# Kernel tuning notes

Measured on AMD Instinct MI355X. Metric: run time of the kernel, lower is better.

The kernel has to match this reference:

```python
import jax, jax.numpy as jnp
import numpy as np
from jax.ops import segment_sum

N_NODES = 50000
N_EDGES = 800000
D = 64
N_LAYERS = 3
N_GRAPHS = 512


def setup_inputs() -> dict:
    key = jax.random.key(0)
    k1, k2, k3, k4 = jax.random.split(key, 4)
    x = jax.random.normal(k1, (N_NODES, D), dtype=jnp.float32)
    Ws = jax.random.normal(k2, (N_LAYERS, D, D), dtype=jnp.float32) * (1.0 / np.sqrt(D))
    bs = jnp.zeros((N_LAYERS, D), dtype=jnp.float32)
    edge_index = jax.random.randint(k3, (2, N_EDGES), 0, N_NODES, dtype=jnp.int64)
    batch = jnp.sort(jax.random.randint(k4, (N_NODES,), 0, N_GRAPHS, dtype=jnp.int64))
    return {"x": x, "Ws": Ws, "bs": bs, "edge_index": edge_index, "batch": batch}


def _gcn_layer(h, W, b, src, dst, n_nodes, dinv):
    # h: [N, D] -> linear transform then normalized aggregation (PyG GCNConv,
    # add_self_loops=True, symmetric normalization)
    h = h @ W  # [N, D]
    norm = dinv[src] * dinv[dst]  # [E]
    agg = segment_sum(h[src] * norm[:, None], dst, num_segments=n_nodes)
    # self-loop contribution: norm_ii = dinv[i]^2, weight 1
    agg = agg + h * (dinv * dinv)[:, None]
    return agg + b


def reference(x, Ws, bs, edge_index, batch):
    src, dst = edge_index[0], edge_index[1]
    n_nodes = x.shape[0]
    # degree with self-loops (edge weight 1): deg[i] = in-degree + 1
    deg = segment_sum(jnp.ones((src.shape[0],), dtype=x.dtype), dst,
                      num_segments=n_nodes) + 1.0
    dinv = jax.lax.rsqrt(deg)
    h = x
    for l in range(Ws.shape[0]):
        h = _gcn_layer(h, Ws[l], bs[l], src, dst, n_nodes, dinv)
    # global_mean_pool over batch index
    sums = segment_sum(h, batch, num_segments=N_GRAPHS)  # [G, D]
    counts = segment_sum(jnp.ones((n_nodes,), dtype=h.dtype), batch,
                         num_segments=N_GRAPHS)
    return sums / jnp.maximum(counts, 1.0)[:, None]
```

## Files before the change

kernel.cpp:

```cpp
#include <hip/hip_runtime.h>

#define N_NODES 50000
#define N_EDGES 800000
#define D 64
#define N_LAYERS 3
#define N_GRAPHS 512

#define NB 196
#define BCAP 5120
#define P3_CHUNK 2048
#define N_P3_WG ((N_EDGES + P3_CHUNK - 1) / P3_CHUNK)
#define LPAD 68

__global__ __launch_bounds__(256) void gbounds_kernel(
    const int* __restrict__ batch, int* __restrict__ gstart,
    int* __restrict__ bucket_fill, int nN) {
    int i = blockIdx.x * 256 + threadIdx.x;
    if (blockIdx.x == 0 && threadIdx.x < NB) bucket_fill[threadIdx.x] = 0;
    if (i >= nN) return;
    int b = batch[i];
    int prev = (i == 0) ? -1 : batch[i - 1];
    for (int g = prev + 1; g <= b; ++g) gstart[g] = i;
    if (i == nN - 1) {
        for (int g = b + 1; g <= N_GRAPHS; ++g) gstart[g] = nN;
    }
}


__global__ __launch_bounds__(256) void bucket_scatter_kernel(
    const int* __restrict__ src, const int* __restrict__ dst,
    int* __restrict__ bucket_fill, int* __restrict__ bucketArr, int nE) {
    __shared__ int hist[NB], base[NB], cur[NB];
    int tid = threadIdx.x;
    if (tid < NB) hist[tid] = 0;
    __syncthreads();
    int s8[8], d8[8];
    bool v8[8];
    int ebase = blockIdx.x * P3_CHUNK + tid;
    #pragma unroll
    for (int i = 0; i < 8; ++i) {
        int e = ebase + i * 256;
        v8[i] = (e < nE);
        if (v8[i]) {
            s8[i] = src[e];
            d8[i] = dst[e];
            atomicAdd(&hist[d8[i] >> 8], 1);
        }
    }
    __syncthreads();
    if (tid < NB) {
        base[tid] = atomicAdd(&bucket_fill[tid], hist[tid]);
        cur[tid] = 0;
    }
    __syncthreads();
    #pragma unroll
    for (int i = 0; i < 8; ++i) {
        if (v8[i]) {
            int b = d8[i] >> 8;
            int r = atomicAdd(&cur[b], 1);
            int pos = base[b] + r;
            if (pos < BCAP)
                bucketArr[b * BCAP + pos] = (s8[i] & 0xFFFF) | ((d8[i] & 0xFF) << 16);
        }
    }
}

__global__ __launch_bounds__(256) void bucket_csr_kernel(
    const int* __restrict__ bucket_fill, const int* __restrict__ bucketArr,
    const float* __restrict__ x,
    int* __restrict__ offsets, int* __restrict__ csr_src,
    float* __restrict__ dinv, float* __restrict__ v0) {
    __shared__ int bsum[256];
    __shared__ int ldeg[256], lsc[256], lcur[256];
    int b = blockIdx.x;
    int tid = threadIdx.x;
    int ownb = (tid < NB) ? bucket_fill[tid] : 0;
    bsum[tid] = ownb;
    __syncthreads();
    for (int off = 1; off < 256; off <<= 1) {
        int v = (tid >= off) ? bsum[tid - off] : 0;
        __syncthreads();
        bsum[tid] += v;
        __syncthreads();
    }
    int cbase = (b == 0) ? 0 : bsum[b - 1];
    if (b == NB - 1 && tid == 0) offsets[N_NODES] = bsum[NB - 1];
    int cnt = min(bucket_fill[b], BCAP);
    const int* seg = bucketArr + b * BCAP;
    ldeg[tid] = 0;
    __syncthreads();
    for (int e = tid; e < cnt; e += 256)
        atomicAdd(&ldeg[(seg[e] >> 16) & 0xFF], 1);
    __syncthreads();
    int own = ldeg[tid];
    lsc[tid] = own;
    __syncthreads();
    for (int off = 1; off < 256; off <<= 1) {
        int v = (tid >= off) ? lsc[tid - off] : 0;
        __syncthreads();
        lsc[tid] += v;
        __syncthreads();
    }
    int excl = lsc[tid] - own;
    int node = b * 256 + tid;
    if (node < N_NODES) {
        float di = rsqrtf((float)own + 1.0f);
        offsets[node] = cbase + excl;
        dinv[node] = di;
        const float4* xr = (const float4*)&x[(size_t)node * D];
        float4* vr = (float4*)&v0[(size_t)node * D];
        #pragma unroll
        for (int i = 0; i < D / 4; ++i) {
            float4 t = xr[i];
            t.x *= di; t.y *= di; t.z *= di; t.w *= di;
            vr[i] = t;
        }
    }
    lcur[tid] = cbase + excl;
    __syncthreads();
    for (int e = tid; e < cnt; e += 256) {
        int p = seg[e];
        int pos = atomicAdd(&lcur[(p >> 16) & 0xFF], 1);
        csr_src[pos] = p & 0xFFFF;
    }
}

__global__ __launch_bounds__(256) void fused_layer_kernel(
    const int* __restrict__ offsets, const int* __restrict__ csr_src,
    const float* __restrict__ v, const float* __restrict__ dinv,
    const float* __restrict__ W, const float* __restrict__ b,
    float* __restrict__ vout, int last) {
    __shared__ float A[16][LPAD];
    __shared__ float Wl[D][LPAD];
    int tid = threadIdx.x;
    #pragma unroll
    for (int i = 0; i < 4; ++i) {
        int idx4 = tid + i * 256;
        int r = idx4 >> 4;
        int c4 = (idx4 & 15) << 2;
        *(float4*)&Wl[r][c4] = *(const float4*)&W[r * D + c4];
    }
    int wave = tid >> 6;
    int lane = tid & 63;
    int grp = lane >> 4;
    int q4  = (lane & 15) << 2;
    int t0 = blockIdx.x * 16;
    #pragma unroll
    for (int rr = 0; rr < 4; ++rr) {
        int r = rr * 4 + wave;
        int t = t0 + r;
        int beg = offsets[t];
        int end = offsets[t + 1];
        float4 acc0 = make_float4(0.f, 0.f, 0.f, 0.f);
        float4 acc1 = make_float4(0.f, 0.f, 0.f, 0.f);
        int e = beg + grp;
        for (; e + 4 < end; e += 8) {
            int s0 = csr_src[e];
            int s1 = csr_src[e + 4];
            float4 v0 = *(const float4*)&v[(size_t)s0 * D + q4];
            float4 v1 = *(const float4*)&v[(size_t)s1 * D + q4];
            acc0.x += v0.x; acc0.y += v0.y; acc0.z += v0.z; acc0.w += v0.w;
            acc1.x += v1.x; acc1.y += v1.y; acc1.z += v1.z; acc1.w += v1.w;
        }
        if (e < end) {
            int s0 = csr_src[e];
            float4 v0 = *(const float4*)&v[(size_t)s0 * D + q4];
            acc0.x += v0.x; acc0.y += v0.y; acc0.z += v0.z; acc0.w += v0.w;
        }
        float4 acc = make_float4(acc0.x + acc1.x, acc0.y + acc1.y,
                                 acc0.z + acc1.z, acc0.w + acc1.w);
        #pragma unroll
        for (int m = 16; m < 64; m <<= 1) {
            acc.x += __shfl_xor(acc.x, m);
            acc.y += __shfl_xor(acc.y, m);
            acc.z += __shfl_xor(acc.z, m);
            acc.w += __shfl_xor(acc.w, m);
        }
        if (grp == 0) {
            float4 self = *(const float4*)&v[(size_t)t * D + q4];
            float dt = dinv[t];
            float4 a;
            a.x = (acc.x + self.x) * dt;
            a.y = (acc.y + self.y) * dt;
            a.z = (acc.z + self.z) * dt;
            a.w = (acc.w + self.w) * dt;
            *(float4*)&A[r][q4] = a;
        }
    }
    __syncthreads();
    int r  = tid >> 4;
    int c0 = (tid & 15) << 2;
    float4 acc = make_float4(0.f, 0.f, 0.f, 0.f);
    #pragma unroll
    for (int k = 0; k < D; k += 4) {
        float4 a  = *(float4*)&A[r][k];
        float4 w0 = *(float4*)&Wl[k + 0][c0];
        float4 w1 = *(float4*)&Wl[k + 1][c0];
        float4 w2 = *(float4*)&Wl[k + 2][c0];
        float4 w3 = *(float4*)&Wl[k + 3][c0];
        acc.x += a.x * w0.x + a.y * w1.x + a.z * w2.x + a.w * w3.x;
        acc.y += a.x * w0.y + a.y * w1.y + a.z * w2.y + a.w * w3.y;
        acc.z += a.x * w0.z + a.y * w1.z + a.z * w2.z + a.w * w3.z;
        acc.w += a.x * w0.w + a.y * w1.w + a.z * w2.w + a.w * w3.w;
    }
    int t = t0 + r;
    float4 bb = *(const float4*)&b[c0];
    float4 o;
    o.x = acc.x + bb.x;
    o.y = acc.y + bb.y;
    o.z = acc.z + bb.z;
    o.w = acc.w + bb.w;
    if (!last) {
        float dt = dinv[t];
        o.x *= dt; o.y *= dt; o.z *= dt; o.w *= dt;
    }
    *(float4*)&vout[(size_t)t * D + c0] = o;
}


__global__ __launch_bounds__(256) void pool_kernel(
    const float* __restrict__ h, const int* __restrict__ gstart,
    float* __restrict__ out) {
    __shared__ float sm[4][D];
    int g = blockIdx.x;
    int wave = threadIdx.x >> 6;
    int lane = threadIdx.x & 63;
    int beg = gstart[g];
    int end = gstart[g + 1];
    float acc = 0.f;
    int n = beg + wave;
    for (; n + 12 < end; n += 16) {
        float a0 = h[(size_t)(n)      * D + lane];
        float a1 = h[(size_t)(n + 4)  * D + lane];
        float a2 = h[(size_t)(n + 8)  * D + lane];
        float a3 = h[(size_t)(n + 12) * D + lane];
        acc += a0 + a1 + a2 + a3;
    }
    for (; n < end; n += 4)
        acc += h[(size_t)n * D + lane];
    sm[wave][lane] = acc;
    __syncthreads();
    if (wave == 0) {
        float s = sm[0][lane] + sm[1][lane] + sm[2][lane] + sm[3][lane];
        float cnt = (float)(end - beg);
        out[g * D + lane] = s / fmaxf(cnt, 1.0f);
    }
}


#define WS_ALIGN(p) ((char*)(((size_t)(p) + 255) & ~(size_t)255))

extern "C" void kernel_launch(void* const* d_in, const int* in_sizes, int n_in,
                              void* d_out, int out_size, void* d_ws, size_t ws_size,
                              hipStream_t stream) {
    const float* x     = (const float*)d_in[0];
    const float* Ws    = (const float*)d_in[1];
    const float* bs    = (const float*)d_in[2];
    const int*   edge  = (const int*)d_in[3];
    const int*   batch = (const int*)d_in[4];
    const int* src = edge;
    const int* dst = edge + N_EDGES;
    float* out = (float*)d_out;

    char* p = (char*)d_ws;
    int* offsets     = (int*)p;      p = WS_ALIGN(p + sizeof(int) * (N_NODES + 1));
    int* csr_src     = (int*)p;      p = WS_ALIGN(p + sizeof(int) * N_EDGES);
    int* bucket_fill = (int*)p;      p = WS_ALIGN(p + sizeof(int) * NB);
    int* gstart      = (int*)p;      p = WS_ALIGN(p + sizeof(int) * (N_GRAPHS + 1));
    float* dinv      = (float*)p;    p = WS_ALIGN(p + sizeof(float) * N_NODES);
    float* B1        = (float*)p;    p = WS_ALIGN(p + sizeof(float) * (size_t)N_NODES * D);
    float* B2        = (float*)p;
    int* bucketArr = (int*)B2;

    gbounds_kernel<<<(N_NODES + 255) / 256, 256, 0, stream>>>(batch, gstart, bucket_fill, N_NODES);
    bucket_scatter_kernel<<<N_P3_WG, 256, 0, stream>>>(src, dst, bucket_fill, bucketArr, N_EDGES);
    bucket_csr_kernel<<<NB, 256, 0, stream>>>(bucket_fill, bucketArr, x,
                                              offsets, csr_src, dinv, B1);

    fused_layer_kernel<<<N_NODES / 16, 256, 0, stream>>>(
        offsets, csr_src, B1, dinv, Ws + 0 * (size_t)D * D, bs + 0 * D, B2, 0);
    fused_layer_kernel<<<N_NODES / 16, 256, 0, stream>>>(
        offsets, csr_src, B2, dinv, Ws + 1 * (size_t)D * D, bs + 1 * D, B1, 0);
    fused_layer_kernel<<<N_NODES / 16, 256, 0, stream>>>(
        offsets, csr_src, B1, dinv, Ws + 2 * (size_t)D * D, bs + 2 * D, B2, 1);

    pool_kernel<<<N_GRAPHS, 256, 0, stream>>>(B2, gstart, out);
}
```

Measured before the change: 160.2 us.

## Compute per-row matvec in-wave via shuffles, dropping shared A tile and barrier

```diff
diff --git a/kernel.cpp b/kernel.cpp
--- a/kernel.cpp
+++ b/kernel.cpp
@@ -130,7 +130,6 @@
     const float* __restrict__ v, const float* __restrict__ dinv,
     const float* __restrict__ W, const float* __restrict__ b,
     float* __restrict__ vout, int last) {
-    __shared__ float A[16][LPAD];
     __shared__ float Wl[D][LPAD];
     int tid = threadIdx.x;
     #pragma unroll
@@ -140,15 +139,16 @@
         int c4 = (idx4 & 15) << 2;
         *(float4*)&Wl[r][c4] = *(const float4*)&W[r * D + c4];
     }
+    __syncthreads();
     int wave = tid >> 6;
     int lane = tid & 63;
     int grp = lane >> 4;
     int q4  = (lane & 15) << 2;
     int t0 = blockIdx.x * 16;
+    float4 bb = *(const float4*)&b[q4];
     #pragma unroll
     for (int rr = 0; rr < 4; ++rr) {
-        int r = rr * 4 + wave;
-        int t = t0 + r;
+        int t = t0 + rr * 4 + wave;
         int beg = offsets[t];
         int end = offsets[t + 1];
         float4 acc0 = make_float4(0.f, 0.f, 0.f, 0.f);
@@ -176,45 +176,45 @@
             acc.z += __shfl_xor(acc.z, m);
             acc.w += __shfl_xor(acc.w, m);
         }
+        float dt = dinv[t];
+        float4 self = *(const float4*)&v[(size_t)t * D + q4];
+        float4 a;
+        a.x = (acc.x + self.x) * dt;
+        a.y = (acc.y + self.y) * dt;
+        a.z = (acc.z + self.z) * dt;
+        a.w = (acc.w + self.w) * dt;
+        float4 p = make_float4(0.f, 0.f, 0.f, 0.f);
+        #pragma unroll
+        for (int i = 0; i < 16; ++i) {
+            int srcl = grp * 4 + (i >> 2);
+            float ak;
+            if ((i & 3) == 0)      ak = __shfl(a.x, srcl);
+            else if ((i & 3) == 1) ak = __shfl(a.y, srcl);
+            else if ((i & 3) == 2) ak = __shfl(a.z, srcl);
+            else                   ak = __shfl(a.w, srcl);
+            int k = grp * 16 + i;
+            float4 w = *(float4*)&Wl[k][q4];
+            p.x += ak * w.x; p.y += ak * w.y; p.z += ak * w.z; p.w += ak * w.w;
+        }
+        #pragma unroll
+        for (int m = 16; m < 64; m <<= 1) {
+            p.x += __shfl_xor(p.x, m);
+            p.y += __shfl_xor(p.y, m);
+            p.z += __shfl_xor(p.z, m);
+            p.w += __shfl_xor(p.w, m);
+        }
         if (grp == 0) {
-            float4 self = *(const float4*)&v[(size_t)t * D + q4];
-            float dt = dinv[t];
-            float4 a;
-            a.x = (acc.x + self.x) * dt;
-            a.y = (acc.y + self.y) * dt;
-            a.z = (acc.z + self.z) * dt;
-            a.w = (acc.w + self.w) * dt;
-            *(float4*)&A[r][q4] = a;
-        }
-    }
-    __syncthreads();
-    int r  = tid >> 4;
-    int c0 = (tid & 15) << 2;
-    float4 acc = make_float4(0.f, 0.f, 0.f, 0.f);
-    #pragma unroll
-    for (int k = 0; k < D; k += 4) {
-        float4 a  = *(float4*)&A[r][k];
-        float4 w0 = *(float4*)&Wl[k + 0][c0];
-        float4 w1 = *(float4*)&Wl[k + 1][c0];
-        float4 w2 = *(float4*)&Wl[k + 2][c0];
-        float4 w3 = *(float4*)&Wl[k + 3][c0];
-        acc.x += a.x * w0.x + a.y * w1.x + a.z * w2.x + a.w * w3.x;
-        acc.y += a.x * w0.y + a.y * w1.y + a.z * w2.y + a.w * w3.y;
-        acc.z += a.x * w0.z + a.y * w1.z + a.z * w2.z + a.w * w3.z;
-        acc.w += a.x * w0.w + a.y * w1.w + a.z * w2.w + a.w * w3.w;
-    }
-    int t = t0 + r;
-    float4 bb = *(const float4*)&b[c0];
-    float4 o;
-    o.x = acc.x + bb.x;
-    o.y = acc.y + bb.y;
-    o.z = acc.z + bb.z;
-    o.w = acc.w + bb.w;
-    if (!last) {
-        float dt = dinv[t];
-        o.x *= dt; o.y *= dt; o.z *= dt; o.w *= dt;
-    }
-    *(float4*)&vout[(size_t)t * D + c0] = o;
+            float4 o;
+            o.x = p.x + bb.x;
+            o.y = p.y + bb.y;
+            o.z = p.z + bb.z;
+            o.w = p.w + bb.w;
+            if (!last) {
+                o.x *= dt; o.y *= dt; o.z *= dt; o.w *= dt;
+            }
+            *(float4*)&vout[(size_t)t * D + q4] = o;
+        }
+    }
 }
 
 
```

Result: slower. 201.6 us (+25.8%).
